# Optimization experiments

Measured on AMD Instinct MI355X. Metric: run time of the kernel, lower is better.

The kernel has to match this reference:

```python
import jax, jax.numpy as jnp
import numpy as np

B, T, D, M, H = 1, 256, 512, 64, 8
HD = D // H              # head_dim = 64
IN = 2 * HD + 2 * M      # crossing_net input dim = 256
HID = D // 2             # crossing_net hidden = 256


def setup_inputs() -> dict:
    key = jax.random.key(0)
    ks = jax.random.split(key, 14)
    s = 0.02
    return {
        "x": jax.random.normal(ks[0], (B, T, D), jnp.float32),
        "coords": jax.random.normal(ks[1], (B, T, M), jnp.float32),
        "Wq": jax.random.normal(ks[2], (D, D), jnp.float32) * s,
        "Wk": jax.random.normal(ks[3], (D, D), jnp.float32) * s,
        "Wv": jax.random.normal(ks[4], (D, D), jnp.float32) * s,
        "Wo": jax.random.normal(ks[5], (D, D), jnp.float32) * s,
        "W1": jax.random.normal(ks[6], (IN, HID), jnp.float32) * s,
        "b1": jnp.zeros((HID,), jnp.float32),
        "W2": jax.random.normal(ks[7], (HID, 2), jnp.float32) * s,
        "b2": jnp.zeros((2,), jnp.float32),
        "W3": jax.random.normal(ks[8], (D, D), jnp.float32) * s,
        "b3": jnp.zeros((D,), jnp.float32),
        "W4": jax.random.normal(ks[9], (D, D), jnp.float32) * s,
        "b4": jnp.zeros((D,), jnp.float32),
    }


def reference(x, coords, Wq, Wk, Wv, Wo, W1, b1, W2, b2, W3, b3, W4, b4):
    b, t, d = x.shape
    m = coords.shape[-1]
    hd = d // H
    # projections -> (B, H, T, HD)
    q = (x @ Wq).reshape(b, t, H, hd).transpose(0, 2, 1, 3)
    k = (x @ Wk).reshape(b, t, H, hd).transpose(0, 2, 1, 3)
    v = (x @ Wv).reshape(b, t, H, hd).transpose(0, 2, 1, 3)
    # crossing_net layer1 on concat([q_i, k_j, c_i, c_j]) decomposes by blocks of W1:
    W1q, W1k = W1[:hd], W1[hd:2 * hd]
    W1ci, W1cj = W1[2 * hd:2 * hd + m], W1[2 * hd + m:]
    a_i = jnp.einsum('bhid,df->bhif', q, W1q) + jnp.einsum('bim,mf->bif', coords, W1ci)[:, None]
    a_j = jnp.einsum('bhjd,df->bhjf', k, W1k) + jnp.einsum('bjm,mf->bjf', coords, W1cj)[:, None] + b1
    # (B,H,T,T,HID) pairwise hidden, then layer2 -> 2 logits
    h = jax.nn.silu(a_i[:, :, :, None, :] + a_j[:, :, None, :, :])
    z = jnp.einsum('bhijf,fc->bhijc', h, W2) + b2
    crossings = jax.nn.softmax(z, axis=-1)            # (B,H,T,T,2)
    linking = crossings[..., 0] - crossings[..., 1]   # (B,H,T,T)
    scores = linking / np.float32(np.sqrt(hd))
    causal = jnp.triu(jnp.ones((t, t), bool), 1)
    scores = jnp.where(causal, -jnp.inf, scores)
    attn = jax.nn.softmax(scores, axis=-1)
    out = jnp.einsum('bhij,bhjd->bhid', attn, v)
    out = out.transpose(0, 2, 1, 3).reshape(b, t, d)
    out = jax.nn.silu(out @ W3 + b3) @ W4 + b4        # invariant_net
    out = out @ Wo                                    # to_out
    writhe = linking.sum(axis=(-1, -2))               # (B,H)
    linking_mean = jnp.abs(linking).mean()
    return out, writhe, linking_mean
```

## Files before the change

### kernel.cpp

```cpp
#include <hip/hip_runtime.h>
#include <math.h>

#define T_ 256
#define D_ 512
#define M_ 64
#define H_ 8
#define HD_ 64
#define HID_ 256


__global__ __launch_bounds__(256) void qkv_kernel(
    const float* __restrict__ x,
    const float* __restrict__ Wq, const float* __restrict__ Wk,
    const float* __restrict__ Wv, float* __restrict__ y)
{
    __shared__ __align__(16) float As[32][36];
    __shared__ __align__(16) float Bs[32][36];

    const int z = blockIdx.z;
    const float* W = (z == 0) ? Wq : (z == 1) ? Wk : Wv;
    float* C = y + (long)z * (T_ * D_);

    const int tid = threadIdx.x;
    const int tx = tid & 15, ty = tid >> 4;
    const int row0 = blockIdx.y * 32, col0 = blockIdx.x * 32;
    const int r4 = tid >> 3, c4 = tid & 7;

    float acc00 = 0.f, acc01 = 0.f, acc10 = 0.f, acc11 = 0.f;

    for (int k0 = 0; k0 < D_; k0 += 32) {
        *(float4*)&As[r4][c4 * 4] = *(const float4*)(x + (long)(row0 + r4) * D_ + k0 + c4 * 4);
        *(float4*)&Bs[r4][c4 * 4] = *(const float4*)(W + (long)(k0 + r4) * D_ + col0 + c4 * 4);
        __syncthreads();
        #pragma unroll
        for (int kk = 0; kk < 32; ++kk) {
            float a0 = As[ty * 2 + 0][kk];
            float a1 = As[ty * 2 + 1][kk];
            float b0 = Bs[kk][tx * 2 + 0];
            float b1 = Bs[kk][tx * 2 + 1];
            acc00 = fmaf(a0, b0, acc00); acc01 = fmaf(a0, b1, acc01);
            acc10 = fmaf(a1, b0, acc10); acc11 = fmaf(a1, b1, acc11);
        }
        __syncthreads();
    }
    C[(long)(row0 + ty * 2 + 0) * D_ + col0 + tx * 2 + 0] = acc00;
    C[(long)(row0 + ty * 2 + 0) * D_ + col0 + tx * 2 + 1] = acc01;
    C[(long)(row0 + ty * 2 + 1) * D_ + col0 + tx * 2 + 0] = acc10;
    C[(long)(row0 + ty * 2 + 1) * D_ + col0 + tx * 2 + 1] = acc11;
}

__global__ __launch_bounds__(256) void aiaj_kernel(
    const float* __restrict__ y, const float* __restrict__ coords,
    const float* __restrict__ W1, const float* __restrict__ b1,
    float* __restrict__ abuf)
{
    __shared__ __align__(16) float As[32][36];
    __shared__ __align__(16) float Bs[32][36];

    const int z = blockIdx.z;
    const int sel = z >> 3, h = z & 7;
    const float* Ay = y + (long)sel * (T_ * D_) + h * HD_;
    float* C = abuf + (long)z * (T_ * HID_);

    const int tid = threadIdx.x;
    const int tx = tid & 15, ty = tid >> 4;
    const int row0 = blockIdx.y * 32, col0 = blockIdx.x * 32;
    const int r4 = tid >> 3, c4 = tid & 7;

    float acc00 = 0.f, acc01 = 0.f, acc10 = 0.f, acc11 = 0.f;

    for (int k0 = 0; k0 < 128; k0 += 32) {
        if (k0 < 64) {
            *(float4*)&As[r4][c4 * 4] =
                *(const float4*)(Ay + (long)(row0 + r4) * D_ + k0 + c4 * 4);
            *(float4*)&Bs[r4][c4 * 4] =
                *(const float4*)(W1 + (long)(sel * 64 + k0 + r4) * HID_ + col0 + c4 * 4);
        } else {
            *(float4*)&As[r4][c4 * 4] =
                *(const float4*)(coords + (long)(row0 + r4) * M_ + (k0 - 64) + c4 * 4);
            *(float4*)&Bs[r4][c4 * 4] =
                *(const float4*)(W1 + (long)(128 + 64 * sel + k0 - 64 + r4) * HID_ + col0 + c4 * 4);
        }
        __syncthreads();
        #pragma unroll
        for (int kk = 0; kk < 32; ++kk) {
            float a0 = As[ty * 2 + 0][kk];
            float a1 = As[ty * 2 + 1][kk];
            float b0 = Bs[kk][tx * 2 + 0];
            float b1 = Bs[kk][tx * 2 + 1];
            acc00 = fmaf(a0, b0, acc00); acc01 = fmaf(a0, b1, acc01);
            acc10 = fmaf(a1, b0, acc10); acc11 = fmaf(a1, b1, acc11);
        }
        __syncthreads();
    }
    const int c0 = col0 + tx * 2, r0 = row0 + ty * 2;
    float bb0 = (sel == 1) ? b1[c0 + 0] : 0.f;
    float bb1 = (sel == 1) ? b1[c0 + 1] : 0.f;
    C[(long)(r0 + 0) * HID_ + c0 + 0] = acc00 + bb0;
    C[(long)(r0 + 0) * HID_ + c0 + 1] = acc01 + bb1;
    C[(long)(r0 + 1) * HID_ + c0 + 0] = acc10 + bb0;
    C[(long)(r0 + 1) * HID_ + c0 + 1] = acc11 + bb1;
}

#define SILU_ACC(acc, w, aa, bb) \
    { float t_ = (aa) + (bb); \
      float sg_ = __builtin_amdgcn_rcpf(1.f + __expf(-t_)); \
      acc = fmaf((w) * t_, sg_, acc); }

__global__ __launch_bounds__(256) void pairwise_kernel(
    const float* __restrict__ a_i, const float* __restrict__ a_j,
    const float* __restrict__ W2, float* __restrict__ pb)
{
    const int jt = blockIdx.x, it = blockIdx.y, hs = blockIdx.z;
    const int h = hs >> 2, fb = (hs & 3) * 64;
    const int t = threadIdx.x;

    __shared__ __align__(16) float ai_s[32][68];
    __shared__ __align__(16) float aj_s[32][68];
    __shared__ __align__(16) float w2d[64];

    if (t < 64) w2d[t] = W2[(fb + t) * 2 + 0] - W2[(fb + t) * 2 + 1];

    const float* aib = a_i + ((long)h * T_ + it * 32) * HID_ + fb;
    const float* ajb = a_j + ((long)h * T_ + jt * 32) * HID_ + fb;
    #pragma unroll
    for (int l = 0; l < 2; ++l) {
        int idx = t + l * 256;
        int r = idx >> 4, c4 = idx & 15;
        *(float4*)&ai_s[r][c4 * 4] = *(const float4*)(aib + (long)r * HID_ + c4 * 4);
        *(float4*)&aj_s[r][c4 * 4] = *(const float4*)(ajb + (long)r * HID_ + c4 * 4);
    }
    __syncthreads();

    const int ty = t >> 4, tx = t & 15;
    float s00 = 0.f, s01 = 0.f, s10 = 0.f, s11 = 0.f;

    #pragma unroll 4
    for (int f4 = 0; f4 < 16; ++f4) {
        float4 a0 = *(const float4*)&ai_s[ty][f4 * 4];
        float4 a1 = *(const float4*)&ai_s[ty + 16][f4 * 4];
        float4 c0 = *(const float4*)&aj_s[tx][f4 * 4];
        float4 c1 = *(const float4*)&aj_s[tx + 16][f4 * 4];
        float4 w  = *(const float4*)&w2d[f4 * 4];
        SILU_ACC(s00, w.x, a0.x, c0.x); SILU_ACC(s01, w.x, a0.x, c1.x);
        SILU_ACC(s10, w.x, a1.x, c0.x); SILU_ACC(s11, w.x, a1.x, c1.x);
        SILU_ACC(s00, w.y, a0.y, c0.y); SILU_ACC(s01, w.y, a0.y, c1.y);
        SILU_ACC(s10, w.y, a1.y, c0.y); SILU_ACC(s11, w.y, a1.y, c1.y);
        SILU_ACC(s00, w.z, a0.z, c0.z); SILU_ACC(s01, w.z, a0.z, c1.z);
        SILU_ACC(s10, w.z, a1.z, c0.z); SILU_ACC(s11, w.z, a1.z, c1.z);
        SILU_ACC(s00, w.w, a0.w, c0.w); SILU_ACC(s01, w.w, a0.w, c1.w);
        SILU_ACC(s10, w.w, a1.w, c0.w); SILU_ACC(s11, w.w, a1.w, c1.w);
    }

    const int gi0 = it * 32 + ty, gi1 = gi0 + 16;
    const int gj0 = jt * 32 + tx, gj1 = gj0 + 16;
    float* pbh = pb + (long)hs * (T_ * T_);
    pbh[(long)gi0 * T_ + gj0] = s00;
    pbh[(long)gi0 * T_ + gj1] = s01;
    pbh[(long)gi1 * T_ + gj0] = s10;
    pbh[(long)gi1 * T_ + gj1] = s11;
}

__global__ __launch_bounds__(512) void attn_kernel(
    const float* __restrict__ pb, const float* __restrict__ yv,
    const float* __restrict__ b2, float* __restrict__ o,
    float* __restrict__ parts)
{
    const int i = blockIdx.x, t = threadIdx.x;
    const int w = t >> 6, lane = t & 63;

    __shared__ float p[8][256];
    __shared__ float psc[8];

    const float b2d = b2[0] - b2[1];

    const float* pb0 = pb + ((long)(4 * w + 0) * T_ + i) * T_;
    const float* pb1 = pb + ((long)(4 * w + 1) * T_ + i) * T_;
    const float* pb2 = pb + ((long)(4 * w + 2) * T_ + i) * T_;
    const float* pb3 = pb + ((long)(4 * w + 3) * T_ + i) * T_;
    float sv[4];
    float mx = -1e30f, wsum = 0.f, asum = 0.f;
    #pragma unroll
    for (int r = 0; r < 4; ++r) {
        int j = lane + r * 64;
        float s = ((pb0[j] + pb1[j]) + (pb2[j] + pb3[j])) + b2d;
        float as = fabsf(s);
        float e = __expf(-as);
        float tv = (1.f - e) * __builtin_amdgcn_rcpf(1.f + e);
        float lk = (s < 0.f) ? -tv : tv;
        wsum += lk; asum += fabsf(lk);
        float sc = (j <= i) ? lk * 0.125f : -1e30f;
        sv[r] = sc; mx = fmaxf(mx, sc);
    }
    #pragma unroll
    for (int off = 32; off > 0; off >>= 1) mx = fmaxf(mx, __shfl_xor(mx, off));
    float sum = 0.f;
    #pragma unroll
    for (int r = 0; r < 4; ++r) {
        int j = lane + r * 64;
        float e = (j <= i) ? __expf(sv[r] - mx) : 0.f;
        p[w][j] = e; sum += e;
    }
    #pragma unroll
    for (int off = 32; off > 0; off >>= 1) {
        sum  += __shfl_xor(sum, off);
        wsum += __shfl_xor(wsum, off);
        asum += __shfl_xor(asum, off);
    }
    if (lane == 0) {
        psc[w] = __builtin_amdgcn_rcpf(sum);
        parts[((long)i * 8 + w) * 2 + 0] = wsum;
        parts[((long)i * 8 + w) * 2 + 1] = asum;
    }
    __syncthreads();

    const float pinv = psc[w];
    const float* vb = yv + t;
    float a0 = 0.f, a1 = 0.f, a2 = 0.f, a3 = 0.f;
    float a4 = 0.f, a5 = 0.f, a6 = 0.f, a7 = 0.f;
    int j = 0;
    for (; j + 7 <= i; j += 8) {
        a0 = fmaf(p[w][j + 0], vb[(long)(j + 0) * D_], a0);
        a1 = fmaf(p[w][j + 1], vb[(long)(j + 1) * D_], a1);
        a2 = fmaf(p[w][j + 2], vb[(long)(j + 2) * D_], a2);
        a3 = fmaf(p[w][j + 3], vb[(long)(j + 3) * D_], a3);
        a4 = fmaf(p[w][j + 4], vb[(long)(j + 4) * D_], a4);
        a5 = fmaf(p[w][j + 5], vb[(long)(j + 5) * D_], a5);
        a6 = fmaf(p[w][j + 6], vb[(long)(j + 6) * D_], a6);
        a7 = fmaf(p[w][j + 7], vb[(long)(j + 7) * D_], a7);
    }
    for (; j <= i; ++j) a0 = fmaf(p[w][j], vb[(long)j * D_], a0);
    o[(long)i * D_ + t] = (((a0 + a1) + (a2 + a3)) + ((a4 + a5) + (a6 + a7))) * pinv;
}

__global__ __launch_bounds__(256) void epA_kernel(
    const float* __restrict__ o, const float* __restrict__ W3,
    float* __restrict__ hbuf)
{
    __shared__ __align__(16) float As[32][36];
    __shared__ __align__(16) float Bs[32][36];

    const int z = blockIdx.z;
    float* C = hbuf + (long)z * (T_ * D_);
    const int tid = threadIdx.x;
    const int tx = tid & 15, ty = tid >> 4;
    const int row0 = blockIdx.y * 32, col0 = blockIdx.x * 32;
    const int r4 = tid >> 3, c4 = tid & 7;

    float acc00 = 0.f, acc01 = 0.f, acc10 = 0.f, acc11 = 0.f;

    for (int k0 = z * 256; k0 < z * 256 + 256; k0 += 32) {
        *(float4*)&As[r4][c4 * 4] = *(const float4*)(o + (long)(row0 + r4) * D_ + k0 + c4 * 4);
        *(float4*)&Bs[r4][c4 * 4] = *(const float4*)(W3 + (long)(k0 + r4) * D_ + col0 + c4 * 4);
        __syncthreads();
        #pragma unroll
        for (int kk = 0; kk < 32; ++kk) {
            float a0 = As[ty * 2 + 0][kk];
            float a1 = As[ty * 2 + 1][kk];
            float b0 = Bs[kk][tx * 2 + 0];
            float b1 = Bs[kk][tx * 2 + 1];
            acc00 = fmaf(a0, b0, acc00); acc01 = fmaf(a0, b1, acc01);
            acc10 = fmaf(a1, b0, acc10); acc11 = fmaf(a1, b1, acc11);
        }
        __syncthreads();
    }
    C[(long)(row0 + ty * 2 + 0) * D_ + col0 + tx * 2 + 0] = acc00;
    C[(long)(row0 + ty * 2 + 0) * D_ + col0 + tx * 2 + 1] = acc01;
    C[(long)(row0 + ty * 2 + 1) * D_ + col0 + tx * 2 + 0] = acc10;
    C[(long)(row0 + ty * 2 + 1) * D_ + col0 + tx * 2 + 1] = acc11;
}

__global__ __launch_bounds__(256) void epB_kernel(
    const float* __restrict__ hbuf, const float* __restrict__ b3,
    const float* __restrict__ W4, float* __restrict__ gbuf)
{
    __shared__ __align__(16) float As[32][36];
    __shared__ __align__(16) float Bs[32][36];

    const int z = blockIdx.z;
    const float* h0 = hbuf;
    const float* h1 = hbuf + (T_ * D_);
    float* C = gbuf + (long)z * (T_ * D_);
    const int tid = threadIdx.x;
    const int tx = tid & 15, ty = tid >> 4;
    const int row0 = blockIdx.y * 32, col0 = blockIdx.x * 32;
    const int r4 = tid >> 3, c4 = tid & 7;

    float acc00 = 0.f, acc01 = 0.f, acc10 = 0.f, acc11 = 0.f;

    for (int k0 = z * 256; k0 < z * 256 + 256; k0 += 32) {
        {
            long off = (long)(row0 + r4) * D_ + k0 + c4 * 4;
            float4 v0 = *(const float4*)(h0 + off);
            float4 v1 = *(const float4*)(h1 + off);
            float4 bb = *(const float4*)(b3 + k0 + c4 * 4);
            float4 g;
            g.x = v0.x + v1.x + bb.x; g.y = v0.y + v1.y + bb.y;
            g.z = v0.z + v1.z + bb.z; g.w = v0.w + v1.w + bb.w;
            g.x = g.x * __builtin_amdgcn_rcpf(1.f + __expf(-g.x));
            g.y = g.y * __builtin_amdgcn_rcpf(1.f + __expf(-g.y));
            g.z = g.z * __builtin_amdgcn_rcpf(1.f + __expf(-g.z));
            g.w = g.w * __builtin_amdgcn_rcpf(1.f + __expf(-g.w));
            *(float4*)&As[r4][c4 * 4] = g;
        }
        *(float4*)&Bs[r4][c4 * 4] = *(const float4*)(W4 + (long)(k0 + r4) * D_ + col0 + c4 * 4);
        __syncthreads();
        #pragma unroll
        for (int kk = 0; kk < 32; ++kk) {
            float a0 = As[ty * 2 + 0][kk];
            float a1 = As[ty * 2 + 1][kk];
            float b0 = Bs[kk][tx * 2 + 0];
            float b1 = Bs[kk][tx * 2 + 1];
            acc00 = fmaf(a0, b0, acc00); acc01 = fmaf(a0, b1, acc01);
            acc10 = fmaf(a1, b0, acc10); acc11 = fmaf(a1, b1, acc11);
        }
        __syncthreads();
    }
    C[(long)(row0 + ty * 2 + 0) * D_ + col0 + tx * 2 + 0] = acc00;
    C[(long)(row0 + ty * 2 + 0) * D_ + col0 + tx * 2 + 1] = acc01;
    C[(long)(row0 + ty * 2 + 1) * D_ + col0 + tx * 2 + 0] = acc10;
    C[(long)(row0 + ty * 2 + 1) * D_ + col0 + tx * 2 + 1] = acc11;
}

__global__ __launch_bounds__(256) void epC_kernel(
    const float* __restrict__ gbuf, const float* __restrict__ b4,
    const float* __restrict__ Wo, float* __restrict__ out,
    const float* __restrict__ parts, float* __restrict__ tailo)
{
    __shared__ __align__(16) float As[32][36];
    __shared__ __align__(16) float Bs[32][36];

    const float* g0 = gbuf;
    const float* g1 = gbuf + (T_ * D_);
    const int tid = threadIdx.x;
    const int tx = tid & 15, ty = tid >> 4;
    const int row0 = blockIdx.y * 32, col0 = blockIdx.x * 32;
    const int r4 = tid >> 3, c4 = tid & 7;

    float acc00 = 0.f, acc01 = 0.f, acc10 = 0.f, acc11 = 0.f;

    for (int k0 = 0; k0 < D_; k0 += 32) {
        {
            long off = (long)(row0 + r4) * D_ + k0 + c4 * 4;
            float4 v0 = *(const float4*)(g0 + off);
            float4 v1 = *(const float4*)(g1 + off);
            float4 bb = *(const float4*)(b4 + k0 + c4 * 4);
            float4 g;
            g.x = v0.x + v1.x + bb.x; g.y = v0.y + v1.y + bb.y;
            g.z = v0.z + v1.z + bb.z; g.w = v0.w + v1.w + bb.w;
            *(float4*)&As[r4][c4 * 4] = g;
        }
        *(float4*)&Bs[r4][c4 * 4] = *(const float4*)(Wo + (long)(k0 + r4) * D_ + col0 + c4 * 4);
        __syncthreads();
        #pragma unroll
        for (int kk = 0; kk < 32; ++kk) {
            float a0 = As[ty * 2 + 0][kk];
            float a1 = As[ty * 2 + 1][kk];
            float b0 = Bs[kk][tx * 2 + 0];
            float b1 = Bs[kk][tx * 2 + 1];
            acc00 = fmaf(a0, b0, acc00); acc01 = fmaf(a0, b1, acc01);
            acc10 = fmaf(a1, b0, acc10); acc11 = fmaf(a1, b1, acc11);
        }
        __syncthreads();
    }
    out[(long)(row0 + ty * 2 + 0) * D_ + col0 + tx * 2 + 0] = acc00;
    out[(long)(row0 + ty * 2 + 0) * D_ + col0 + tx * 2 + 1] = acc01;
    out[(long)(row0 + ty * 2 + 1) * D_ + col0 + tx * 2 + 0] = acc10;
    out[(long)(row0 + ty * 2 + 1) * D_ + col0 + tx * 2 + 1] = acc11;

    if (blockIdx.x == 0 && blockIdx.y == 0 && tid < 64) {
        const int lane = tid;
        if (lane < 8) {
            float wsum = 0.f;
            for (int i = 0; i < 256; ++i) wsum += parts[((long)i * 8 + lane) * 2 + 0];
            tailo[lane] = wsum;
        }
        float a = 0.f;
        for (int idx = lane; idx < 2048; idx += 64) a += parts[(long)idx * 2 + 1];
        #pragma unroll
        for (int off = 32; off > 0; off >>= 1) a += __shfl_xor(a, off);
        if (lane == 0) tailo[8] = a / (float)(H_ * T_ * T_);
    }
}

extern "C" void kernel_launch(void* const* d_in, const int* in_sizes, int n_in,
                              void* d_out, int out_size, void* d_ws, size_t ws_size,
                              hipStream_t stream)
{
    const float* x      = (const float*)d_in[0];
    const float* coords = (const float*)d_in[1];
    const float* Wq     = (const float*)d_in[2];
    const float* Wk     = (const float*)d_in[3];
    const float* Wv     = (const float*)d_in[4];
    const float* Wo     = (const float*)d_in[5];
    const float* W1     = (const float*)d_in[6];
    const float* b1     = (const float*)d_in[7];
    const float* W2     = (const float*)d_in[8];
    const float* b2     = (const float*)d_in[9];
    const float* W3     = (const float*)d_in[10];
    const float* b3     = (const float*)d_in[11];
    const float* W4     = (const float*)d_in[12];
    const float* b4     = (const float*)d_in[13];
    float* out = (float*)d_out;

    float* ws = (float*)d_ws;
    float* y     = ws;
    float* ai    = ws + 393216;
    float* aj    = ws + 917504;
    float* pb    = ws + 1441792;
    float* o     = ws + 3538944;
    float* hb    = ws + 3670016;
    float* gb    = ws + 3932160;
    float* parts = ws + 4194304;

    qkv_kernel<<<dim3(16, 8, 3), dim3(256), 0, stream>>>(x, Wq, Wk, Wv, y);

    aiaj_kernel<<<dim3(8, 8, 16), dim3(256), 0, stream>>>(y, coords, W1, b1, ai);

    pairwise_kernel<<<dim3(8, 8, 32), dim3(256), 0, stream>>>(ai, aj, W2, pb);

    attn_kernel<<<dim3(T_), dim3(512), 0, stream>>>(pb, y + 2 * (T_ * D_), b2, o, parts);

    epA_kernel<<<dim3(16, 8, 2), dim3(256), 0, stream>>>(o, W3, hb);
    epB_kernel<<<dim3(16, 8, 2), dim3(256), 0, stream>>>(hb, b3, W4, gb);
    epC_kernel<<<dim3(16, 8), dim3(256), 0, stream>>>(gb, b4, Wo, out, parts, out + 131072);
}
```

Baseline: 119.4 us.

## Fold W4 and b4 into Wo and merge the tail GEMMs into fewer kernels

Precomputes W4·Wo and b4·Wo inside the first kernel, alongside the QKV projection, so the epilogue becomes one split-K GEMM with W3 followed by a single fused SiLU GEMM instead of three chained GEMMs. epA now uses a 4-way K split and reuses the pairwise buffer as scratch. This removes one kernel launch and one full-size intermediate GEMM pass from the serial tail. In exchange the first kernel does an extra weight-only 512x512x512 product on every call and the summation order changes slightly.

```diff
diff --git a/kernel.cpp b/kernel.cpp
--- a/kernel.cpp
+++ b/kernel.cpp
@@ -9,66 +9,93 @@
 #define HID_ 256
 
 
-__global__ __launch_bounds__(256) void qkv_kernel(
+#define SILU_ACC(acc, w, aa, bb) \
+    { float t_ = (aa) + (bb); \
+      float sg_ = __builtin_amdgcn_rcpf(1.f + __expf(-t_)); \
+      acc = fmaf((w) * t_, sg_, acc); }
+
+#define GEMM_INNER \
+    _Pragma("unroll") \
+    for (int kk = 0; kk < 32; ++kk) { \
+        float a0 = As[ty * 2 + 0][kk]; \
+        float a1 = As[ty * 2 + 1][kk]; \
+        float b0 = Bs[kk][tx * 2 + 0]; \
+        float b1 = Bs[kk][tx * 2 + 1]; \
+        a00 = fmaf(a0, b0, a00); a01 = fmaf(a0, b1, a01); \
+        a10 = fmaf(a1, b0, a10); a11 = fmaf(a1, b1, a11); }
+
+__global__ __launch_bounds__(256) void k1_kernel(
     const float* __restrict__ x,
     const float* __restrict__ Wq, const float* __restrict__ Wk,
-    const float* __restrict__ Wv, float* __restrict__ y)
+    const float* __restrict__ Wv, const float* __restrict__ W4,
+    const float* __restrict__ Wo, const float* __restrict__ b4,
+    float* __restrict__ y, float* __restrict__ W4o, float* __restrict__ b4o)
 {
     __shared__ __align__(16) float As[32][36];
     __shared__ __align__(16) float Bs[32][36];
 
+    const int job = blockIdx.x;
+    const int tid = threadIdx.x;
+    const int tx = tid & 15, ty = tid >> 4;
+    const int r4 = tid >> 3, c4 = tid & 7;
+
+    if (job < 640) {
+        const float* A;
+        const float* B;
+        float* C;
+        int row0, col0;
+        if (job < 384) {
+            const int z = job >> 7, rem = job & 127;
+            row0 = (rem >> 4) << 5; col0 = (rem & 15) << 5;
+            A = x;
+            B = (z == 0) ? Wq : (z == 1) ? Wk : Wv;
+            C = y + (long)z * (T_ * D_);
+        } else {
+            const int idx = job - 384;
+            row0 = (idx >> 4) << 5; col0 = (idx & 15) << 5;
+            A = W4; B = Wo; C = W4o;
+        }
+        float a00 = 0.f, a01 = 0.f, a10 = 0.f, a11 = 0.f;
+        for (int k0 = 0; k0 < D_; k0 += 32) {
+            *(float4*)&As[r4][c4 * 4] = *(const float4*)(A + (long)(row0 + r4) * D_ + k0 + c4 * 4);
+            *(float4*)&Bs[r4][c4 * 4] = *(const float4*)(B + (long)(k0 + r4) * D_ + col0 + c4 * 4);
+            __syncthreads();
+            GEMM_INNER
+            __syncthreads();
+        }
+        C[(long)(row0 + ty * 2 + 0) * D_ + col0 + tx * 2 + 0] = a00;
+        C[(long)(row0 + ty * 2 + 0) * D_ + col0 + tx * 2 + 1] = a01;
+        C[(long)(row0 + ty * 2 + 1) * D_ + col0 + tx * 2 + 0] = a10;
+        C[(long)(row0 + ty * 2 + 1) * D_ + col0 + tx * 2 + 1] = a11;
+    } else {
+        const int c = (job - 640) * 256 + tid;
+        float s = 0.f;
+        for (int k = 0; k < D_; k += 4) {
+            s = fmaf(b4[k + 0], Wo[(long)(k + 0) * D_ + c], s);
+            s = fmaf(b4[k + 1], Wo[(long)(k + 1) * D_ + c], s);
+            s = fmaf(b4[k + 2], Wo[(long)(k + 2) * D_ + c], s);
+            s = fmaf(b4[k + 3], Wo[(long)(k + 3) * D_ + c], s);
+        }
+        b4o[c] = s;
+    }
+}
+
+__global__ __launch_bounds__(256) void aiaj_kernel(
+    const float* __restrict__ y, const float* __restrict__ coords,
+    const float* __restrict__ W1, const float* __restrict__ b1,
+    float* __restrict__ abuf)
+{
+    __shared__ __align__(16) float As[32][36];
+    __shared__ __align__(16) float Bs[32][36];
     const int z = blockIdx.z;
-    const float* W = (z == 0) ? Wq : (z == 1) ? Wk : Wv;
-    float* C = y + (long)z * (T_ * D_);
-
+    const int sel = z >> 3, h = z & 7;
+    const float* Ay = y + (long)sel * (T_ * D_) + h * HD_;
+    float* C = abuf + (long)z * (T_ * HID_);
     const int tid = threadIdx.x;
     const int tx = tid & 15, ty = tid >> 4;
     const int row0 = blockIdx.y * 32, col0 = blockIdx.x * 32;
     const int r4 = tid >> 3, c4 = tid & 7;
-
-    float acc00 = 0.f, acc01 = 0.f, acc10 = 0.f, acc11 = 0.f;
-
-    for (int k0 = 0; k0 < D_; k0 += 32) {
-        *(float4*)&As[r4][c4 * 4] = *(const float4*)(x + (long)(row0 + r4) * D_ + k0 + c4 * 4);
-        *(float4*)&Bs[r4][c4 * 4] = *(const float4*)(W + (long)(k0 + r4) * D_ + col0 + c4 * 4);
-        __syncthreads();
-        #pragma unroll
-        for (int kk = 0; kk < 32; ++kk) {
-            float a0 = As[ty * 2 + 0][kk];
-            float a1 = As[ty * 2 + 1][kk];
-            float b0 = Bs[kk][tx * 2 + 0];
-            float b1 = Bs[kk][tx * 2 + 1];
-            acc00 = fmaf(a0, b0, acc00); acc01 = fmaf(a0, b1, acc01);
-            acc10 = fmaf(a1, b0, acc10); acc11 = fmaf(a1, b1, acc11);
-        }
-        __syncthreads();
-    }
-    C[(long)(row0 + ty * 2 + 0) * D_ + col0 + tx * 2 + 0] = acc00;
-    C[(long)(row0 + ty * 2 + 0) * D_ + col0 + tx * 2 + 1] = acc01;
-    C[(long)(row0 + ty * 2 + 1) * D_ + col0 + tx * 2 + 0] = acc10;
-    C[(long)(row0 + ty * 2 + 1) * D_ + col0 + tx * 2 + 1] = acc11;
-}
-
-__global__ __launch_bounds__(256) void aiaj_kernel(
-    const float* __restrict__ y, const float* __restrict__ coords,
-    const float* __restrict__ W1, const float* __restrict__ b1,
-    float* __restrict__ abuf)
-{
-    __shared__ __align__(16) float As[32][36];
-    __shared__ __align__(16) float Bs[32][36];
-
-    const int z = blockIdx.z;
-    const int sel = z >> 3, h = z & 7;
-    const float* Ay = y + (long)sel * (T_ * D_) + h * HD_;
-    float* C = abuf + (long)z * (T_ * HID_);
-
-    const int tid = threadIdx.x;
-    const int tx = tid & 15, ty = tid >> 4;
-    const int row0 = blockIdx.y * 32, col0 = blockIdx.x * 32;
-    const int r4 = tid >> 3, c4 = tid & 7;
-
-    float acc00 = 0.f, acc01 = 0.f, acc10 = 0.f, acc11 = 0.f;
-
+    float a00 = 0.f, a01 = 0.f, a10 = 0.f, a11 = 0.f;
     for (int k0 = 0; k0 < 128; k0 += 32) {
         if (k0 < 64) {
             *(float4*)&As[r4][c4 * 4] =
@@ -82,30 +109,17 @@
                 *(const float4*)(W1 + (long)(128 + 64 * sel + k0 - 64 + r4) * HID_ + col0 + c4 * 4);
         }
         __syncthreads();
-        #pragma unroll
-        for (int kk = 0; kk < 32; ++kk) {
-            float a0 = As[ty * 2 + 0][kk];
-            float a1 = As[ty * 2 + 1][kk];
-            float b0 = Bs[kk][tx * 2 + 0];
-            float b1 = Bs[kk][tx * 2 + 1];
-            acc00 = fmaf(a0, b0, acc00); acc01 = fmaf(a0, b1, acc01);
-            acc10 = fmaf(a1, b0, acc10); acc11 = fmaf(a1, b1, acc11);
-        }
+        GEMM_INNER
         __syncthreads();
     }
     const int c0 = col0 + tx * 2, r0 = row0 + ty * 2;
     float bb0 = (sel == 1) ? b1[c0 + 0] : 0.f;
     float bb1 = (sel == 1) ? b1[c0 + 1] : 0.f;
-    C[(long)(r0 + 0) * HID_ + c0 + 0] = acc00 + bb0;
-    C[(long)(r0 + 0) * HID_ + c0 + 1] = acc01 + bb1;
-    C[(long)(r0 + 1) * HID_ + c0 + 0] = acc10 + bb0;
-    C[(long)(r0 + 1) * HID_ + c0 + 1] = acc11 + bb1;
-}
-
-#define SILU_ACC(acc, w, aa, bb) \
-    { float t_ = (aa) + (bb); \
-      float sg_ = __builtin_amdgcn_rcpf(1.f + __expf(-t_)); \
-      acc = fmaf((w) * t_, sg_, acc); }
+    C[(long)(r0 + 0) * HID_ + c0 + 0] = a00 + bb0;
+    C[(long)(r0 + 0) * HID_ + c0 + 1] = a01 + bb1;
+    C[(long)(r0 + 1) * HID_ + c0 + 0] = a10 + bb0;
+    C[(long)(r0 + 1) * HID_ + c0 + 1] = a11 + bb1;
+}
 
 __global__ __launch_bounds__(256) void pairwise_kernel(
     const float* __restrict__ a_i, const float* __restrict__ a_j,
@@ -114,13 +128,10 @@
     const int jt = blockIdx.x, it = blockIdx.y, hs = blockIdx.z;
     const int h = hs >> 2, fb = (hs & 3) * 64;
     const int t = threadIdx.x;
-
     __shared__ __align__(16) float ai_s[32][68];
     __shared__ __align__(16) float aj_s[32][68];
     __shared__ __align__(16) float w2d[64];
-
     if (t < 64) w2d[t] = W2[(fb + t) * 2 + 0] - W2[(fb + t) * 2 + 1];
-
     const float* aib = a_i + ((long)h * T_ + it * 32) * HID_ + fb;
     const float* ajb = a_j + ((long)h * T_ + jt * 32) * HID_ + fb;
     #pragma unroll
@@ -131,10 +142,8 @@
         *(float4*)&aj_s[r][c4 * 4] = *(const float4*)(ajb + (long)r * HID_ + c4 * 4);
     }
     __syncthreads();
-
     const int ty = t >> 4, tx = t & 15;
     float s00 = 0.f, s01 = 0.f, s10 = 0.f, s11 = 0.f;
-
     #pragma unroll 4
     for (int f4 = 0; f4 < 16; ++f4) {
         float4 a0 = *(const float4*)&ai_s[ty][f4 * 4];
@@ -151,7 +160,6 @@
         SILU_ACC(s00, w.w, a0.w, c0.w); SILU_ACC(s01, w.w, a0.w, c1.w);
         SILU_ACC(s10, w.w, a1.w, c0.w); SILU_ACC(s11, w.w, a1.w, c1.w);
     }
-
     const int gi0 = it * 32 + ty, gi1 = gi0 + 16;
     const int gj0 = jt * 32 + tx, gj1 = gj0 + 16;
     float* pbh = pb + (long)hs * (T_ * T_);
@@ -168,12 +176,9 @@
 {
     const int i = blockIdx.x, t = threadIdx.x;
     const int w = t >> 6, lane = t & 63;
-
     __shared__ float p[8][256];
     __shared__ float psc[8];
-
     const float b2d = b2[0] - b2[1];
-
     const float* pb0 = pb + ((long)(4 * w + 0) * T_ + i) * T_;
     const float* pb1 = pb + ((long)(4 * w + 1) * T_ + i) * T_;
     const float* pb2 = pb + ((long)(4 * w + 2) * T_ + i) * T_;
@@ -213,7 +218,6 @@
         parts[((long)i * 8 + w) * 2 + 1] = asum;
     }
     __syncthreads();
-
     const float pinv = psc[w];
     const float* vb = yv + t;
     float a0 = 0.f, a1 = 0.f, a2 = 0.f, a3 = 0.f;
@@ -239,134 +243,68 @@
 {
     __shared__ __align__(16) float As[32][36];
     __shared__ __align__(16) float Bs[32][36];
-
     const int z = blockIdx.z;
     float* C = hbuf + (long)z * (T_ * D_);
     const int tid = threadIdx.x;
     const int tx = tid & 15, ty = tid >> 4;
     const int row0 = blockIdx.y * 32, col0 = blockIdx.x * 32;
     const int r4 = tid >> 3, c4 = tid & 7;
-
-    float acc00 = 0.f, acc01 = 0.f, acc10 = 0.f, acc11 = 0.f;
-
-    for (int k0 = z * 256; k0 < z * 256 + 256; k0 += 32) {
+    float a00 = 0.f, a01 = 0.f, a10 = 0.f, a11 = 0.f;
+    for (int k0 = z * 128; k0 < z * 128 + 128; k0 += 32) {
         *(float4*)&As[r4][c4 * 4] = *(const float4*)(o + (long)(row0 + r4) * D_ + k0 + c4 * 4);
         *(float4*)&Bs[r4][c4 * 4] = *(const float4*)(W3 + (long)(k0 + r4) * D_ + col0 + c4 * 4);
         __syncthreads();
-        #pragma unroll
-        for (int kk = 0; kk < 32; ++kk) {
-            float a0 = As[ty * 2 + 0][kk];
-            float a1 = As[ty * 2 + 1][kk];
-            float b0 = Bs[kk][tx * 2 + 0];
-            float b1 = Bs[kk][tx * 2 + 1];
-            acc00 = fmaf(a0, b0, acc00); acc01 = fmaf(a0, b1, acc01);
-            acc10 = fmaf(a1, b0, acc10); acc11 = fmaf(a1, b1, acc11);
-        }
-        __syncthreads();
-    }
-    C[(long)(row0 + ty * 2 + 0) * D_ + col0 + tx * 2 + 0] = acc00;
-    C[(long)(row0 + ty * 2 + 0) * D_ + col0 + tx * 2 + 1] = acc01;
-    C[(long)(row0 + ty * 2 + 1) * D_ + col0 + tx * 2 + 0] = acc10;
-    C[(long)(row0 + ty * 2 + 1) * D_ + col0 + tx * 2 + 1] = acc11;
-}
-
-__global__ __launch_bounds__(256) void epB_kernel(
+        GEMM_INNER
+        __syncthreads();
+    }
+    C[(long)(row0 + ty * 2 + 0) * D_ + col0 + tx * 2 + 0] = a00;
+    C[(long)(row0 + ty * 2 + 0) * D_ + col0 + tx * 2 + 1] = a01;
+    C[(long)(row0 + ty * 2 + 1) * D_ + col0 + tx * 2 + 0] = a10;
+    C[(long)(row0 + ty * 2 + 1) * D_ + col0 + tx * 2 + 1] = a11;
+}
+
+__global__ __launch_bounds__(256) void epF_kernel(
     const float* __restrict__ hbuf, const float* __restrict__ b3,
-    const float* __restrict__ W4, float* __restrict__ gbuf)
+    const float* __restrict__ W4o, const float* __restrict__ b4o,
+    float* __restrict__ out, const float* __restrict__ parts,
+    float* __restrict__ tailo)
 {
     __shared__ __align__(16) float As[32][36];
     __shared__ __align__(16) float Bs[32][36];
-
-    const int z = blockIdx.z;
-    const float* h0 = hbuf;
-    const float* h1 = hbuf + (T_ * D_);
-    float* C = gbuf + (long)z * (T_ * D_);
     const int tid = threadIdx.x;
     const int tx = tid & 15, ty = tid >> 4;
     const int row0 = blockIdx.y * 32, col0 = blockIdx.x * 32;
     const int r4 = tid >> 3, c4 = tid & 7;
-
-    float acc00 = 0.f, acc01 = 0.f, acc10 = 0.f, acc11 = 0.f;
-
-    for (int k0 = z * 256; k0 < z * 256 + 256; k0 += 32) {
+    float a00 = 0.f, a01 = 0.f, a10 = 0.f, a11 = 0.f;
+    for (int k0 = 0; k0 < D_; k0 += 32) {
         {
             long off = (long)(row0 + r4) * D_ + k0 + c4 * 4;
-            float4 v0 = *(const float4*)(h0 + off);
-            float4 v1 = *(const float4*)(h1 + off);
+            float4 v0 = *(const float4*)(hbuf + off);
+            float4 v1 = *(const float4*)(hbuf + 131072 + off);
+            float4 v2 = *(const float4*)(hbuf + 262144 + off);
+            float4 v3 = *(const float4*)(hbuf + 393216 + off);
             float4 bb = *(const float4*)(b3 + k0 + c4 * 4);
             float4 g;
-            g.x = v0.x + v1.x + bb.x; g.y = v0.y + v1.y + bb.y;
-            g.z = v0.z + v1.z + bb.z; g.w = v0.w + v1.w + bb.w;
+            g.x = ((v0.x + v1.x) + (v2.x + v3.x)) + bb.x;
+            g.y = ((v0.y + v1.y) + (v2.y + v3.y)) + bb.y;
+            g.z = ((v0.z + v1.z) + (v2.z + v3.z)) + bb.z;
+            g.w = ((v0.w + v1.w) + (v2.w + v3.w)) + bb.w;
             g.x = g.x * __builtin_amdgcn_rcpf(1.f + __expf(-g.x));
             g.y = g.y * __builtin_amdgcn_rcpf(1.f + __expf(-g.y));
             g.z = g.z * __builtin_amdgcn_rcpf(1.f + __expf(-g.z));
             g.w = g.w * __builtin_amdgcn_rcpf(1.f + __expf(-g.w));
             *(float4*)&As[r4][c4 * 4] = g;
         }
-        *(float4*)&Bs[r4][c4 * 4] = *(const float4*)(W4 + (long)(k0 + r4) * D_ + col0 + c4 * 4);
-        __syncthreads();
-        #pragma unroll
-        for (int kk = 0; kk < 32; ++kk) {
-            float a0 = As[ty * 2 + 0][kk];
-            float a1 = As[ty * 2 + 1][kk];
-            float b0 = Bs[kk][tx * 2 + 0];
-            float b1 = Bs[kk][tx * 2 + 1];
-            acc00 = fmaf(a0, b0, acc00); acc01 = fmaf(a0, b1, acc01);
-            acc10 = fmaf(a1, b0, acc10); acc11 = fmaf(a1, b1, acc11);
-        }
-        __syncthreads();
-    }
-    C[(long)(row0 + ty * 2 + 0) * D_ + col0 + tx * 2 + 0] = acc00;
-    C[(long)(row0 + ty * 2 + 0) * D_ + col0 + tx * 2 + 1] = acc01;
-    C[(long)(row0 + ty * 2 + 1) * D_ + col0 + tx * 2 + 0] = acc10;
-    C[(long)(row0 + ty * 2 + 1) * D_ + col0 + tx * 2 + 1] = acc11;
-}
-
-__global__ __launch_bounds__(256) void epC_kernel(
-    const float* __restrict__ gbuf, const float* __restrict__ b4,
-    const float* __restrict__ Wo, float* __restrict__ out,
-    const float* __restrict__ parts, float* __restrict__ tailo)
-{
-    __shared__ __align__(16) float As[32][36];
-    __shared__ __align__(16) float Bs[32][36];
-
-    const float* g0 = gbuf;
-    const float* g1 = gbuf + (T_ * D_);
-    const int tid = threadIdx.x;
-    const int tx = tid & 15, ty = tid >> 4;
-    const int row0 = blockIdx.y * 32, col0 = blockIdx.x * 32;
-    const int r4 = tid >> 3, c4 = tid & 7;
-
-    float acc00 = 0.f, acc01 = 0.f, acc10 = 0.f, acc11 = 0.f;
-
-    for (int k0 = 0; k0 < D_; k0 += 32) {
-        {
-            long off = (long)(row0 + r4) * D_ + k0 + c4 * 4;
-            float4 v0 = *(const float4*)(g0 + off);
-            float4 v1 = *(const float4*)(g1 + off);
-            float4 bb = *(const float4*)(b4 + k0 + c4 * 4);
-            float4 g;
-            g.x = v0.x + v1.x + bb.x; g.y = v0.y + v1.y + bb.y;
-            g.z = v0.z + v1.z + bb.z; g.w = v0.w + v1.w + bb.w;
-            *(float4*)&As[r4][c4 * 4] = g;
-        }
-        *(float4*)&Bs[r4][c4 * 4] = *(const float4*)(Wo + (long)(k0 + r4) * D_ + col0 + c4 * 4);
-        __syncthreads();
-        #pragma unroll
-        for (int kk = 0; kk < 32; ++kk) {
-            float a0 = As[ty * 2 + 0][kk];
-            float a1 = As[ty * 2 + 1][kk];
-            float b0 = Bs[kk][tx * 2 + 0];
-            float b1 = Bs[kk][tx * 2 + 1];
-            acc00 = fmaf(a0, b0, acc00); acc01 = fmaf(a0, b1, acc01);
-            acc10 = fmaf(a1, b0, acc10); acc11 = fmaf(a1, b1, acc11);
-        }
-        __syncthreads();
-    }
-    out[(long)(row0 + ty * 2 + 0) * D_ + col0 + tx * 2 + 0] = acc00;
-    out[(long)(row0 + ty * 2 + 0) * D_ + col0 + tx * 2 + 1] = acc01;
-    out[(long)(row0 + ty * 2 + 1) * D_ + col0 + tx * 2 + 0] = acc10;
-    out[(long)(row0 + ty * 2 + 1) * D_ + col0 + tx * 2 + 1] = acc11;
+        *(float4*)&Bs[r4][c4 * 4] = *(const float4*)(W4o + (long)(k0 + r4) * D_ + col0 + c4 * 4);
+        __syncthreads();
+        GEMM_INNER
+        __syncthreads();
+    }
+    const int c0 = col0 + tx * 2;
+    out[(long)(row0 + ty * 2 + 0) * D_ + c0 + 0] = a00 + b4o[c0 + 0];
+    out[(long)(row0 + ty * 2 + 0) * D_ + c0 + 1] = a01 + b4o[c0 + 1];
+    out[(long)(row0 + ty * 2 + 1) * D_ + c0 + 0] = a10 + b4o[c0 + 0];
+    out[(long)(row0 + ty * 2 + 1) * D_ + c0 + 1] = a11 + b4o[c0 + 1];
 
     if (blockIdx.x == 0 && blockIdx.y == 0 && tid < 64) {
         const int lane = tid;
@@ -409,11 +347,13 @@
     float* aj    = ws + 917504;
     float* pb    = ws + 1441792;
     float* o     = ws + 3538944;
-    float* hb    = ws + 3670016;
-    float* gb    = ws + 3932160;
-    float* parts = ws + 4194304;
-
-    qkv_kernel<<<dim3(16, 8, 3), dim3(256), 0, stream>>>(x, Wq, Wk, Wv, y);
+    float* parts = ws + 3670016;
+    float* W4o   = ws + 3674112;
+    float* b4o   = ws + 3936256;
+    float* hb    = pb;
+
+    k1_kernel<<<dim3(642), dim3(256), 0, stream>>>(x, Wq, Wk, Wv, W4, Wo, b4,
+                                                   y, W4o, b4o);
 
     aiaj_kernel<<<dim3(8, 8, 16), dim3(256), 0, stream>>>(y, coords, W1, b1, ai);
 
@@ -421,7 +361,8 @@
 
     attn_kernel<<<dim3(T_), dim3(512), 0, stream>>>(pb, y + 2 * (T_ * D_), b2, o, parts);
 
-    epA_kernel<<<dim3(16, 8, 2), dim3(256), 0, stream>>>(o, W3, hb);
-    epB_kernel<<<dim3(16, 8, 2), dim3(256), 0, stream>>>(hb, b3, W4, gb);
-    epC_kernel<<<dim3(16, 8), dim3(256), 0, stream>>>(gb, b4, Wo, out, parts, out + 131072);
-}
+    epA_kernel<<<dim3(16, 8, 4), dim3(256), 0, stream>>>(o, W3, hb);
+
+    epF_kernel<<<dim3(16, 8), dim3(256), 0, stream>>>(hb, b3, W4o, b4o, out,
+                                                      parts, out + 131072);
+}
```

Measured after the change: 117.3 us. About the same (-1.8%).
